# Kernel optimization log

Hardware: AMD Instinct MI355X
Metric: run time of the kernel (lower is better)

Reference implementation:

```python
import jax, jax.numpy as jnp
import numpy as np

B, T_ENC, ENC, DEC, MEL = 32, 1024, 1024, 1024, 80


def setup_inputs() -> dict:
    key = jax.random.key(0)
    ks = jax.random.split(key, 10)
    s = lambda k, shape, sc=1.0: (jax.random.normal(k, shape, dtype=jnp.float32) * sc)
    return {
        "prev_mel_frame": s(ks[0], (B, MEL)),
        "encoder_outputs": s(ks[1], (B, T_ENC, ENC)),
        "h": s(ks[2], (B, DEC)),
        "c": s(ks[3], (B, DEC)),
        # AdditiveAttention learned scale vector (use_scale=True default)
        "attn_scale": s(ks[4], (ENC,), 0.05),
        # LSTMCell params: input dim = MEL + ENC, gates order i, f, c, o (Keras)
        "kernel": s(ks[5], (MEL + ENC, 4 * DEC), 0.02),
        "rec_kernel": s(ks[6], (DEC, 4 * DEC), 0.02),
        "bias": s(ks[7], (4 * DEC,), 0.02),
        # Dense projection to mel
        "proj_w": s(ks[8], (DEC, MEL), 0.02),
        "proj_b": s(ks[9], (MEL,), 0.02),
    }


def reference(prev_mel_frame, encoder_outputs, h, c,
              attn_scale, kernel, rec_kernel, bias, proj_w, proj_b):
    # Additive (Bahdanau) attention: scores[b,t] = sum_d scale_d * tanh(h[b,d] + enc[b,t,d])
    feat = jnp.tanh(h[:, None, :] + encoder_outputs)          # [B, T, D]
    scores = jnp.einsum("btd,d->bt", feat, attn_scale)         # [B, T]
    attn = jax.nn.softmax(scores, axis=-1)
    context = jnp.einsum("bt,btd->bd", attn, encoder_outputs)  # [B, ENC]

    # LSTMCell step on concat([prev_mel, context])
    x = jnp.concatenate([prev_mel_frame, context], axis=-1)    # [B, MEL+ENC]
    z = x @ kernel + h @ rec_kernel + bias                     # [B, 4*DEC]
    i, f, g, o = jnp.split(z, 4, axis=-1)
    i = jax.nn.sigmoid(i)
    f = jax.nn.sigmoid(f)
    o = jax.nn.sigmoid(o)
    c_new = f * c + i * jnp.tanh(g)
    h_new = o * jnp.tanh(c_new)

    mel_frame = h_new @ proj_w + proj_b                        # [B, MEL]
    return mel_frame, h_new, c_new
```

## Files before the change

### kernel.cpp

```cpp
#include <hip/hip_runtime.h>

#define BB 32
#define TT 1024
#define ENCD 1024
#define DECD 1024
#define MELD 80
#define KTOT (MELD + ENCD + DECD)
#define NZ (4 * DECD)
#define KCH 136
#define KC 16
#define NTT 32
#define QR 4

__device__ float g_cp[NTT * BB * ENCD];
__device__ float g_m[NTT * BB];
__device__ float g_s[NTT * BB];
__device__ float g_ctx[BB * ENCD];
__device__ float g_zp[KC * BB * NZ];

__device__ __forceinline__ float tanh_fast(float x) {
    return 1.f - __fdividef(2.f, __expf(2.f * x) + 1.f);
}
__device__ __forceinline__ float sigmoid_fast(float x) {
    return __fdividef(1.f, 1.f + __expf(-x));
}

__global__ __launch_bounds__(256, 4) void k_attn(const float* __restrict__ enc,
                                                 const float* __restrict__ hst,
                                                 const float* __restrict__ scale) {
    __shared__ float es[2][QR][ENCD];
    __shared__ float ssc[2][QR];
    int b = blockIdx.x, tc = blockIdx.y;
    int tid = threadIdx.x, w = tid >> 6, lane = tid & 63;
    const float4* hp = (const float4*)(hst + (size_t)b * DECD);
    const float4* sp = (const float4*)scale;
    float4 hr0 = hp[lane], hr1 = hp[lane + 64], hr2 = hp[lane + 128], hr3 = hp[lane + 192];
    float4 sr0 = sp[lane], sr1 = sp[lane + 64], sr2 = sp[lane + 128], sr3 = sp[lane + 192];

    float M = -1e30f, S = 0.f;
    float cx = 0.f, cy = 0.f, cz = 0.f, cw = 0.f;
    const float4* ebase = (const float4*)(enc + ((size_t)b * TT + tc * 32) * ENCD);

    auto stage = [&](int p, int buf) {
        const float4* ep = ebase + (size_t)(p * QR + w) * (ENCD / 4) + lane;
        float4 e0 = ep[0], e1 = ep[64], e2 = ep[128], e3 = ep[192];
        float sc = 0.f;
        sc = fmaf(sr0.x, tanh_fast(hr0.x + e0.x), sc);
        sc = fmaf(sr0.y, tanh_fast(hr0.y + e0.y), sc);
        sc = fmaf(sr0.z, tanh_fast(hr0.z + e0.z), sc);
        sc = fmaf(sr0.w, tanh_fast(hr0.w + e0.w), sc);
        sc = fmaf(sr1.x, tanh_fast(hr1.x + e1.x), sc);
        sc = fmaf(sr1.y, tanh_fast(hr1.y + e1.y), sc);
        sc = fmaf(sr1.z, tanh_fast(hr1.z + e1.z), sc);
        sc = fmaf(sr1.w, tanh_fast(hr1.w + e1.w), sc);
        sc = fmaf(sr2.x, tanh_fast(hr2.x + e2.x), sc);
        sc = fmaf(sr2.y, tanh_fast(hr2.y + e2.y), sc);
        sc = fmaf(sr2.z, tanh_fast(hr2.z + e2.z), sc);
        sc = fmaf(sr2.w, tanh_fast(hr2.w + e2.w), sc);
        sc = fmaf(sr3.x, tanh_fast(hr3.x + e3.x), sc);
        sc = fmaf(sr3.y, tanh_fast(hr3.y + e3.y), sc);
        sc = fmaf(sr3.z, tanh_fast(hr3.z + e3.z), sc);
        sc = fmaf(sr3.w, tanh_fast(hr3.w + e3.w), sc);
#pragma unroll
        for (int off = 32; off; off >>= 1) sc += __shfl_xor(sc, off, 64);
        float4* esr = (float4*)&es[buf][w][0];
        esr[lane] = e0; esr[lane + 64] = e1;
        esr[lane + 128] = e2; esr[lane + 192] = e3;
        if (lane == 0) ssc[buf][w] = sc;
    };
    auto consume = [&](int buf) {
        float s0 = ssc[buf][0], s1 = ssc[buf][1], s2 = ssc[buf][2], s3 = ssc[buf][3];
        float mq = fmaxf(fmaxf(s0, s1), fmaxf(s2, s3));
        float Mn = fmaxf(M, mq);
        float alO = __expf(M - Mn);
        float w0 = __expf(s0 - Mn), w1 = __expf(s1 - Mn);
        float w2 = __expf(s2 - Mn), w3 = __expf(s3 - Mn);
        S = fmaf(S, alO, (w0 + w1) + (w2 + w3));
        M = Mn;
        cx *= alO; cy *= alO; cz *= alO; cw *= alO;
        const float4* col = (const float4*)&es[buf][0][0] + tid;
        float4 e;
        e = col[0];   cx = fmaf(w0, e.x, cx); cy = fmaf(w0, e.y, cy);
                      cz = fmaf(w0, e.z, cz); cw = fmaf(w0, e.w, cw);
        e = col[256]; cx = fmaf(w1, e.x, cx); cy = fmaf(w1, e.y, cy);
                      cz = fmaf(w1, e.z, cz); cw = fmaf(w1, e.w, cw);
        e = col[512]; cx = fmaf(w2, e.x, cx); cy = fmaf(w2, e.y, cy);
                      cz = fmaf(w2, e.z, cz); cw = fmaf(w2, e.w, cw);
        e = col[768]; cx = fmaf(w3, e.x, cx); cy = fmaf(w3, e.y, cy);
                      cz = fmaf(w3, e.z, cz); cw = fmaf(w3, e.w, cw);
    };

    stage(0, 0);
    __syncthreads();
#pragma unroll
    for (int p = 0; p < 8; p++) {
        if (p < 7) stage(p + 1, (p + 1) & 1);
        consume(p & 1);
        __syncthreads();
    }

    float4 r4; r4.x = cx; r4.y = cy; r4.z = cz; r4.w = cw;
    ((float4*)g_cp)[((size_t)tc * BB + b) * (ENCD / 4) + tid] = r4;
    if (tid == 0) { g_m[tc * BB + b] = M; g_s[tc * BB + b] = S; }
}

__global__ __launch_bounds__(128) void k_combine(const float* __restrict__ pb,
                                                 float* __restrict__ out) {
    __shared__ float wgt[NTT];
    int b = blockIdx.x, dq = blockIdx.y, tid = threadIdx.x;
    if (dq == 0 && tid < MELD) out[b * MELD + tid] = pb[tid];
    float M = -1e30f;
#pragma unroll
    for (int tt = 0; tt < NTT; tt++) M = fmaxf(M, g_m[tt * BB + b]);
    float S = 0.f;
#pragma unroll
    for (int tt = 0; tt < NTT; tt++) S += g_s[tt * BB + b] * __expf(g_m[tt * BB + b] - M);
    if (tid < NTT) wgt[tid] = __expf(g_m[tid * BB + b] - M) * __fdividef(1.f, S);
    __syncthreads();
    int d = dq * 128 + tid;
    float acc = 0.f;
#pragma unroll 8
    for (int tt = 0; tt < NTT; tt++)
        acc = fmaf(wgt[tt], g_cp[((size_t)tt * BB + b) * ENCD + d], acc);
    g_ctx[b * ENCD + d] = acc;
}

__global__ __launch_bounds__(256) void k_zmm(const float* __restrict__ pm,
                                             const float* __restrict__ h,
                                             const float* __restrict__ kern,
                                             const float* __restrict__ reck) {
    __shared__ float xs[KCH * 32];
    __shared__ float sacc[32 * 128];
    int jt = blockIdx.x & 31, kc = blockIdx.x >> 5;
    int k0 = kc * KCH;
    int kcount = min(KCH, KTOT - k0);
    int tid = threadIdx.x;
    for (int idx = tid; idx < kcount * 32; idx += 256) {
        int kk = idx >> 5, b = idx & 31;
        int k = k0 + kk;
        float v;
        if (k < MELD)             v = pm[b * MELD + k];
        else if (k < MELD + ENCD) v = g_ctx[b * ENCD + (k - MELD)];
        else                      v = h[b * DECD + (k - MELD - ENCD)];
        xs[idx] = v;
    }
    __syncthreads();
    int jl = tid & 127, kh = tid >> 7;
    int j = jt * 128 + jl;
    int split = (kcount == KCH) ? 72 : 48;
    int kb = kh ? split : 0;
    int ke = kh ? kcount : split;
    float acc[32];
#pragma unroll
    for (int b = 0; b < 32; b++) acc[b] = 0.f;
    for (int kk0 = kb; kk0 < ke; kk0 += 8) {
        float w[8];
#pragma unroll
        for (int i = 0; i < 8; i++) {
            int k = k0 + kk0 + i;
            w[i] = (k < MELD + ENCD) ? kern[(size_t)k * NZ + j]
                                     : reck[(size_t)(k - MELD - ENCD) * NZ + j];
        }
#pragma unroll
        for (int i = 0; i < 8; i++) {
            const float* xr = xs + (kk0 + i) * 32;
#pragma unroll
            for (int b = 0; b < 32; b++) acc[b] = fmaf(xr[b], w[i], acc[b]);
        }
    }
    if (kh) {
#pragma unroll
        for (int b = 0; b < 32; b++) sacc[b * 128 + jl] = acc[b];
    }
    __syncthreads();
    if (!kh) {
#pragma unroll
        for (int b = 0; b < 32; b++)
            g_zp[((size_t)kc * BB + b) * NZ + j] = acc[b] + sacc[b * 128 + jl];
    }
}

__global__ __launch_bounds__(256) void k_gates(const float* __restrict__ bias,
                                               const float* __restrict__ c,
                                               const float* __restrict__ pw,
                                               float* __restrict__ out) {
    __shared__ float sacc[4][4][64];
    __shared__ float lh[64];
    int b = blockIdx.x >> 4, jq = blockIdx.x & 15;
    int jl = threadIdx.x & 63, grp = threadIdx.x >> 6;
    int j = jq * 64 + jl;
    int kc0 = grp * 4;
    int kc1 = kc0 + 4;
    float zi = 0.f, zf = 0.f, zg = 0.f, zo = 0.f;
    for (int kc = kc0; kc < kc1; kc++) {
        const float* zp = g_zp + ((size_t)kc * BB + b) * NZ;
        zi += zp[j];
        zf += zp[1024 + j];
        zg += zp[2048 + j];
        zo += zp[3072 + j];
    }
    sacc[grp][0][jl] = zi; sacc[grp][1][jl] = zf;
    sacc[grp][2][jl] = zg; sacc[grp][3][jl] = zo;
    __syncthreads();
    if (grp == 0) {
        zi = sacc[0][0][jl] + sacc[1][0][jl] + sacc[2][0][jl] + sacc[3][0][jl] + bias[j];
        zf = sacc[0][1][jl] + sacc[1][1][jl] + sacc[2][1][jl] + sacc[3][1][jl] + bias[1024 + j];
        zg = sacc[0][2][jl] + sacc[1][2][jl] + sacc[2][2][jl] + sacc[3][2][jl] + bias[2048 + j];
        zo = sacc[0][3][jl] + sacc[1][3][jl] + sacc[2][3][jl] + sacc[3][3][jl] + bias[3072 + j];
        int idx = b * 1024 + j;
        float cn = sigmoid_fast(zf) * c[idx] + sigmoid_fast(zi) * tanh_fast(zg);
        float hn = sigmoid_fast(zo) * tanh_fast(cn);
        lh[jl] = hn;
        out[2560 + idx] = hn;
        out[35328 + idx] = cn;
    }
    __syncthreads();
    if (threadIdx.x < MELD) {
        int m = threadIdx.x;
        const float* pwp = pw + (size_t)(jq * 64) * MELD + m;
        float acc = 0.f;
#pragma unroll 8
        for (int jj = 0; jj < 64; jj++) acc = fmaf(lh[jj], pwp[jj * MELD], acc);
        atomicAdd(&out[b * MELD + m], acc);
    }
}

extern "C" void kernel_launch(void* const* d_in, const int* in_sizes, int n_in,
                              void* d_out, int out_size, void* d_ws, size_t ws_size,
                              hipStream_t stream) {
    const float* pm   = (const float*)d_in[0];
    const float* enc  = (const float*)d_in[1];
    const float* h    = (const float*)d_in[2];
    const float* c    = (const float*)d_in[3];
    const float* asc  = (const float*)d_in[4];
    const float* kern = (const float*)d_in[5];
    const float* reck = (const float*)d_in[6];
    const float* bias = (const float*)d_in[7];
    const float* pw   = (const float*)d_in[8];
    const float* pb   = (const float*)d_in[9];
    float* out = (float*)d_out;

    k_attn   <<<dim3(32, NTT), 256, 0, stream>>>(enc, h, asc);
    k_combine<<<dim3(32, 8), 128, 0, stream>>>(pb, out);
    k_zmm    <<<512, 256, 0, stream>>>(pm, h, kern, reck);
    k_gates  <<<512, 256, 0, stream>>>(bias, c, pw, out);
}
```

Before: 257.7 us.

## Fold softmax-combine of attention partials into the LSTM gate matmul kernel

Removes the separate combine kernel: each matmul block now computes the per-batch softmax max/sum from partial stats and reduces the partial context vectors only for its own K slice, writing them straight into shared memory. The output bias init moves into the attention kernel, and the shared x tile gets a padded stride of 33. This saves one launch and the g_ctx round trip through global memory. The cost is that 32 column tiles redundantly recompute the same context slice from g_cp, adding global reads and serial work before the matmul starts.

```diff
diff --git a/kernel.cpp b/kernel.cpp
--- a/kernel.cpp
+++ b/kernel.cpp
@@ -11,11 +11,11 @@
 #define KC 16
 #define NTT 32
 #define QR 4
+#define XST 33
 
 __device__ float g_cp[NTT * BB * ENCD];
 __device__ float g_m[NTT * BB];
 __device__ float g_s[NTT * BB];
-__device__ float g_ctx[BB * ENCD];
 __device__ float g_zp[KC * BB * NZ];
 
 __device__ __forceinline__ float tanh_fast(float x) {
@@ -27,11 +27,14 @@
 
 __global__ __launch_bounds__(256, 4) void k_attn(const float* __restrict__ enc,
                                                  const float* __restrict__ hst,
-                                                 const float* __restrict__ scale) {
+                                                 const float* __restrict__ scale,
+                                                 const float* __restrict__ pb,
+                                                 float* __restrict__ out) {
     __shared__ float es[2][QR][ENCD];
     __shared__ float ssc[2][QR];
     int b = blockIdx.x, tc = blockIdx.y;
     int tid = threadIdx.x, w = tid >> 6, lane = tid & 63;
+    if (tc == 0 && tid < MELD) out[b * MELD + tid] = pb[tid];
     const float4* hp = (const float4*)(hst + (size_t)b * DECD);
     const float4* sp = (const float4*)scale;
     float4 hr0 = hp[lane], hr1 = hp[lane + 64], hr2 = hp[lane + 128], hr3 = hp[lane + 192];
@@ -104,47 +107,62 @@
     if (tid == 0) { g_m[tc * BB + b] = M; g_s[tc * BB + b] = S; }
 }
 
-__global__ __launch_bounds__(128) void k_combine(const float* __restrict__ pb,
-                                                 float* __restrict__ out) {
-    __shared__ float wgt[NTT];
-    int b = blockIdx.x, dq = blockIdx.y, tid = threadIdx.x;
-    if (dq == 0 && tid < MELD) out[b * MELD + tid] = pb[tid];
-    float M = -1e30f;
-#pragma unroll
-    for (int tt = 0; tt < NTT; tt++) M = fmaxf(M, g_m[tt * BB + b]);
-    float S = 0.f;
-#pragma unroll
-    for (int tt = 0; tt < NTT; tt++) S += g_s[tt * BB + b] * __expf(g_m[tt * BB + b] - M);
-    if (tid < NTT) wgt[tid] = __expf(g_m[tid * BB + b] - M) * __fdividef(1.f, S);
-    __syncthreads();
-    int d = dq * 128 + tid;
-    float acc = 0.f;
-#pragma unroll 8
-    for (int tt = 0; tt < NTT; tt++)
-        acc = fmaf(wgt[tt], g_cp[((size_t)tt * BB + b) * ENCD + d], acc);
-    g_ctx[b * ENCD + d] = acc;
-}
-
 __global__ __launch_bounds__(256) void k_zmm(const float* __restrict__ pm,
                                              const float* __restrict__ h,
                                              const float* __restrict__ kern,
                                              const float* __restrict__ reck) {
-    __shared__ float xs[KCH * 32];
+    __shared__ float xs[KCH * XST];
     __shared__ float sacc[32 * 128];
+    __shared__ float wgt[32 * 32];
+    __shared__ float sms[64];
     int jt = blockIdx.x & 31, kc = blockIdx.x >> 5;
     int k0 = kc * KCH;
     int kcount = min(KCH, KTOT - k0);
     int tid = threadIdx.x;
+
+    if (tid < 32) {
+        int b = tid;
+        float M = -1e30f;
+#pragma unroll
+        for (int tt = 0; tt < NTT; tt++) M = fmaxf(M, g_m[tt * BB + b]);
+        float S = 0.f;
+#pragma unroll
+        for (int tt = 0; tt < NTT; tt++) S += g_s[tt * BB + b] * __expf(g_m[tt * BB + b] - M);
+        sms[b] = M; sms[32 + b] = __fdividef(1.f, S);
+    }
     for (int idx = tid; idx < kcount * 32; idx += 256) {
         int kk = idx >> 5, b = idx & 31;
         int k = k0 + kk;
-        float v;
-        if (k < MELD)             v = pm[b * MELD + k];
-        else if (k < MELD + ENCD) v = g_ctx[b * ENCD + (k - MELD)];
-        else                      v = h[b * DECD + (k - MELD - ENCD)];
-        xs[idx] = v;
-    }
-    __syncthreads();
+        if (k < MELD)              xs[kk * XST + b] = pm[b * MELD + k];
+        else if (k >= MELD + ENCD) xs[kk * XST + b] = h[b * DECD + (k - MELD - ENCD)];
+    }
+    __syncthreads();
+    for (int i = tid; i < 1024; i += 256) {
+        int b = i & 31, tt = i >> 5;
+        wgt[b * 32 + tt] = __expf(g_m[tt * BB + b] - sms[b]) * sms[32 + b];
+    }
+    __syncthreads();
+    int klo = max(k0, MELD), khi = min(k0 + kcount, MELD + ENCD);
+    int nd = khi - klo;
+    if (nd > 0) {
+        int w = tid >> 6, lane = tid & 63;
+        int d0 = klo - MELD;
+        int kkoff = klo - k0;
+        for (int bb = 0; bb < 8; bb++) {
+            int b = w * 8 + bb;
+            const float* wb = wgt + b * 32;
+            for (int dd = lane; dd < nd; dd += 64) {
+                const float* cpp = g_cp + (size_t)b * ENCD + d0 + dd;
+                float acc = 0.f;
+#pragma unroll 8
+                for (int tt = 0; tt < NTT; tt++)
+                    acc = fmaf(wb[tt], cpp[(size_t)tt * (BB * ENCD)], acc);
+                xs[(kkoff + dd) * XST + b] = acc;
+            }
+        }
+    }
+    __syncthreads();
+
     int jl = tid & 127, kh = tid >> 7;
     int j = jt * 128 + jl;
     int split = (kcount == KCH) ? 72 : 48;
@@ -154,18 +172,18 @@
 #pragma unroll
     for (int b = 0; b < 32; b++) acc[b] = 0.f;
     for (int kk0 = kb; kk0 < ke; kk0 += 8) {
-        float w[8];
+        float wv[8];
 #pragma unroll
         for (int i = 0; i < 8; i++) {
             int k = k0 + kk0 + i;
-            w[i] = (k < MELD + ENCD) ? kern[(size_t)k * NZ + j]
-                                     : reck[(size_t)(k - MELD - ENCD) * NZ + j];
+            wv[i] = (k < MELD + ENCD) ? kern[(size_t)k * NZ + j]
+                                      : reck[(size_t)(k - MELD - ENCD) * NZ + j];
         }
 #pragma unroll
         for (int i = 0; i < 8; i++) {
-            const float* xr = xs + (kk0 + i) * 32;
-#pragma unroll
-            for (int b = 0; b < 32; b++) acc[b] = fmaf(xr[b], w[i], acc[b]);
+            const float* xr = xs + (kk0 + i) * XST;
+#pragma unroll
+            for (int b = 0; b < 32; b++) acc[b] = fmaf(xr[b], wv[i], acc[b]);
         }
     }
     if (kh) {
@@ -240,8 +258,7 @@
     const float* pb   = (const float*)d_in[9];
     float* out = (float*)d_out;
 
-    k_attn   <<<dim3(32, NTT), 256, 0, stream>>>(enc, h, asc);
-    k_combine<<<dim3(32, 8), 128, 0, stream>>>(pb, out);
-    k_zmm    <<<512, 256, 0, stream>>>(pm, h, kern, reck);
-    k_gates  <<<512, 256, 0, stream>>>(bias, c, pw, out);
-}
+    k_attn <<<dim3(32, NTT), 256, 0, stream>>>(enc, h, asc, pb, out);
+    k_zmm  <<<512, 256, 0, stream>>>(pm, h, kern, reck);
+    k_gates<<<512, 256, 0, stream>>>(bias, c, pw, out);
+}
```

Result: slower. 283.1 us (+9.9%).
